# Kernel tuning notes

Hardware: AMD Instinct MI355X
Metric: run time of the kernel (lower is better)

Reference implementation:

```python
import jax, jax.numpy as jnp
import numpy as np

N, E, D, H, G = 50000, 640000, 128, 128, 64
EPS = 1e-5


def gcn_conv(x, row, col, W, b, n):
    # PyG GCNConv: linear transform, symmetric deg^-1/2 normalization (self-loops
    # already appended to row/col), scatter-add aggregation, then bias.
    h = x @ W  # [N, H]
    ones = jnp.ones(row.shape[0], dtype=h.dtype)
    deg = jax.ops.segment_sum(ones, col, num_segments=n)
    dinv = jnp.where(deg > 0, jax.lax.rsqrt(deg), 0.0)
    norm = dinv[row] * dinv[col]                       # [E+N]
    msg = h[row] * norm[:, None]                       # gather + scale
    out = jax.ops.segment_sum(msg, col, num_segments=n)  # scatter-add
    return out + b


def graph_layernorm(x, w, b):
    # PyG LayerNorm(mode='graph') with batch=None: normalize over the whole tensor.
    mu = x.mean()
    xc = x - mu
    std = jnp.sqrt((xc * xc).mean())
    return xc / (std + EPS) * w + b


def setup_inputs() -> dict:
    key = jax.random.key(0)
    ks = jax.random.split(key, 12)
    x = jax.random.normal(ks[0], (N, D), dtype=jnp.float32)
    edge_index = jax.random.randint(ks[1], (2, E), 0, N, dtype=jnp.int64)
    batch = jnp.sort(jax.random.randint(ks[2], (N,), 0, G, dtype=jnp.int64))
    s1 = 1.0 / np.sqrt(D)
    s2 = 1.0 / np.sqrt(H)
    return {
        "x": x,
        "edge_index": edge_index,
        "batch": batch,
        "W1": jax.random.normal(ks[3], (D, H), dtype=jnp.float32) * s1,
        "b1": jnp.zeros((H,), dtype=jnp.float32),
        "ln1_w": jnp.ones((H,), dtype=jnp.float32),
        "ln1_b": jnp.zeros((H,), dtype=jnp.float32),
        "W2": jax.random.normal(ks[4], (H, H), dtype=jnp.float32) * s2,
        "b2": jnp.zeros((H,), dtype=jnp.float32),
        "ln2_w": jnp.ones((H,), dtype=jnp.float32),
        "ln2_b": jnp.zeros((H,), dtype=jnp.float32),
        "fc_w": jax.random.normal(ks[5], (H, 1), dtype=jnp.float32) * s2,
        "fc_b": jnp.zeros((1,), dtype=jnp.float32),
    }


def reference(x, edge_index, batch, W1, b1, ln1_w, ln1_b, W2, b2, ln2_w, ln2_b, fc_w, fc_b):
    n = x.shape[0]
    loops = jnp.arange(n, dtype=edge_index.dtype)
    row = jnp.concatenate([edge_index[0], loops])  # add self-loops
    col = jnp.concatenate([edge_index[1], loops])

    h = gcn_conv(x, row, col, W1, b1, n)
    h = jax.nn.relu(graph_layernorm(h, ln1_w, ln1_b))
    h = gcn_conv(h, row, col, W2, b2, n)
    h = jax.nn.relu(graph_layernorm(h, ln2_w, ln2_b))

    # global_mean_pool over batch segment ids
    sums = jax.ops.segment_sum(h, batch, num_segments=G)          # [G, H]
    cnt = jax.ops.segment_sum(jnp.ones((n,), h.dtype), batch, num_segments=G)
    pooled = sums / jnp.maximum(cnt, 1.0)[:, None]

    logits = pooled @ fc_w + fc_b                                  # [G, 1]
    return jax.nn.sigmoid(logits).squeeze(-1)                      # [G]
```

## Files before the change

kernel.cpp:

```cpp
#include <hip/hip_runtime.h>
#include <math.h>

#define H 128
#define PC 16

typedef _Float16 half8v __attribute__((ext_vector_type(8)));
typedef float floatx4 __attribute__((ext_vector_type(4)));

__device__ __forceinline__ int lower_bound_i(const int* a, int n, int key) {
  int lo = 0, hi = n;
  while (lo < hi) { int mid = (lo + hi) >> 1; if (a[mid] < key) lo = mid + 1; else hi = mid; }
  return lo;
}

__global__ void k_initpack(const float* __restrict__ W1, const float* __restrict__ W2,
                           _Float16* __restrict__ PW1, _Float16* __restrict__ PW2,
                           int* cntE, float* slots, int* esrc, int cap, int n) {
  int b = blockIdx.x;
  int tid = threadIdx.x;
  if (b < 128) {
    int t = b * 256 + tid;
    const float* W = (t < 16384) ? W1 : W2;
    _Float16* PW = (t < 16384) ? PW1 : PW2;
    int u = t & 16383;
    int j = u & 7;
    int nn = (u >> 3) & 15;
    int quad = (u >> 7) & 3;
    int ks = (u >> 9) & 3;
    int ct = (u >> 11) & 7;
    PW[u] = (_Float16)W[(ks * 32 + quad * 8 + j) * H + ct * 16 + nn];
  } else {
    int i = (b - 128) * 256 + tid;
    int stride = 128 * 256;
    for (int j = i; j < n; j += stride) cntE[j] = 0;
    for (int j = i; j < 256; j += stride) slots[j] = 0.f;
    for (int j = i; j < cap; j += stride) esrc[j] = n;
  }
}

__global__ void k_count(const int* __restrict__ col, int* __restrict__ cntE,
                        int* __restrict__ perm, int E) {
  int e = blockIdx.x * blockDim.x + threadIdx.x;
  if (e < E) perm[e] = atomicAdd(&cntE[col[e]], 1);
}

__global__ void k_scan_block(const int* __restrict__ cnt, int* __restrict__ offs,
                             int* __restrict__ bsum, int n) {
  __shared__ int s[256];
  int tid = threadIdx.x;
  int i = blockIdx.x * 256 + tid;
  int v = (i < n) ? ((cnt[i] + 15) & ~15) : 0;
  s[tid] = v;
  __syncthreads();
  for (int d = 1; d < 256; d <<= 1) {
    int t = (tid >= d) ? s[tid - d] : 0;
    __syncthreads();
    s[tid] += t;
    __syncthreads();
  }
  if (i < n) offs[i] = s[tid] - v;
  if (tid == 255) bsum[blockIdx.x] = s[255];
}

__global__ void k_scan_add(int* __restrict__ offs, const int* __restrict__ bsum,
                           const int* __restrict__ cntE, float* __restrict__ dinv, int n) {
  __shared__ int sh[4];
  int tid = threadIdx.x;
  int v = (tid < blockIdx.x) ? bsum[tid] : 0;
#pragma unroll
  for (int o = 32; o > 0; o >>= 1) v += __shfl_xor(v, o, 64);
  if ((tid & 63) == 0) sh[tid >> 6] = v;
  __syncthreads();
  int boff = sh[0] + sh[1] + sh[2] + sh[3];
  int i = blockIdx.x * 256 + tid;
  if (i < n) {
    offs[i] += boff;
    dinv[i] = rsqrtf((float)(cntE[i] + 1));
  }
}

__device__ __forceinline__ void gemm_tile_f32(const float* __restrict__ Xf,
                                              const _Float16* __restrict__ PW,
                                              const float* __restrict__ dinv,
                                              _Float16* __restrict__ O,
                                              int wave, int laneid, int n) {
  int m = laneid & 15;
  int quad = laneid >> 4;
  int r0 = wave * 16;
  int row = r0 + m;
  if (row >= n) row = n - 1;
  floatx4 acc[8] = {};
  const half8v* PB8 = (const half8v*)PW;
#pragma unroll
  for (int ks = 0; ks < 4; ks++) {
    int kb = ks * 32 + quad * 8;
    const float* xr = Xf + (size_t)row * H + kb;
    float4 u0 = *(const float4*)xr;
    float4 u1 = *(const float4*)(xr + 4);
    half8v a;
    a[0] = (_Float16)u0.x; a[1] = (_Float16)u0.y; a[2] = (_Float16)u0.z; a[3] = (_Float16)u0.w;
    a[4] = (_Float16)u1.x; a[5] = (_Float16)u1.y; a[6] = (_Float16)u1.z; a[7] = (_Float16)u1.w;
#pragma unroll
    for (int ct = 0; ct < 8; ct++) {
      half8v b = PB8[((ct * 4 + ks) * 4 + quad) * 16 + m];
      acc[ct] = __builtin_amdgcn_mfma_f32_16x16x32_f16(a, b, acc[ct], 0, 0, 0);
    }
  }
  float dv[4];
#pragma unroll
  for (int reg = 0; reg < 4; reg++) {
    int ro = r0 + quad * 4 + reg;
    dv[reg] = (ro < n) ? dinv[ro] : 0.f;
  }
#pragma unroll
  for (int ct = 0; ct < 8; ct++) {
#pragma unroll
    for (int reg = 0; reg < 4; reg++) {
      int ro = r0 + quad * 4 + reg;
      if (ro < n) O[(size_t)ro * H + ct * 16 + m] = (_Float16)(acc[ct][reg] * dv[reg]);
    }
  }
}

__global__ __launch_bounds__(256) void k_sg1(const int* __restrict__ row, const int* __restrict__ col,
                                             const int* __restrict__ offs, const int* __restrict__ perm,
                                             int* __restrict__ esrc, int E,
                                             const float* __restrict__ Xf,
                                             const _Float16* __restrict__ PW,
                                             const float* __restrict__ dinv,
                                             _Float16* __restrict__ O, int n, int GB) {
  int b = blockIdx.x;
  if (b < GB) {
    if (b == 0 && threadIdx.x < 16) {
      half8v z = {};
      *(half8v*)&O[(size_t)n * H + threadIdx.x * 8] = z;
    }
    int wave = b * 4 + (threadIdx.x >> 6);
    int tiles = (n + 15) >> 4;
    if (wave >= tiles) return;
    gemm_tile_f32(Xf, PW, dinv, O, wave, threadIdx.x & 63, n);
  } else {
    int e = (b - GB) * 256 + threadIdx.x;
    if (e < E) {
      int c = col[e];
      esrc[offs[c] + perm[e]] = row[e];
    }
  }
}

__global__ __launch_bounds__(256) void k_gemm2(const _Float16* __restrict__ Xh,
                                               const _Float16* __restrict__ PW,
                                               const float* __restrict__ lnw,
                                               const float* __restrict__ lnb,
                                               const float* __restrict__ slot, float invM,
                                               const float* __restrict__ dinv,
                                               _Float16* __restrict__ O, int n) {
  if (blockIdx.x == 0 && threadIdx.x < 16) {
    half8v z = {};
    *(half8v*)&O[(size_t)n * H + threadIdx.x * 8] = z;
  }
  int wave = blockIdx.x * 4 + (threadIdx.x >> 6);
  int tiles = (n + 15) >> 4;
  if (wave >= tiles) return;
  int lane = threadIdx.x & 63;
  int m = lane & 15;
  int quad = lane >> 4;
  int r0 = wave * 16;
  int row = r0 + m;
  if (row >= n) row = n - 1;

  float s = slot[lane], q = slot[64 + lane];
#pragma unroll
  for (int o = 32; o > 0; o >>= 1) { s += __shfl_xor(s, o, 64); q += __shfl_xor(q, o, 64); }
  float mu = s * invM;
  float var = fmaxf(q * invM - mu * mu, 0.f);
  float rs = 1.f / (sqrtf(var) + 1e-5f);

  floatx4 acc[8] = {};
  const half8v* PB8 = (const half8v*)PW;
#pragma unroll
  for (int ks = 0; ks < 4; ks++) {
    int kb = ks * 32 + quad * 8;
    half8v hv = *(const half8v*)(Xh + (size_t)row * H + kb);
    float4 w0 = *(const float4*)(lnw + kb);
    float4 w1 = *(const float4*)(lnw + kb + 4);
    float4 c0 = *(const float4*)(lnb + kb);
    float4 c1 = *(const float4*)(lnb + kb + 4);
    half8v a;
    a[0] = (_Float16)fmaxf(((float)hv[0] - mu) * rs * w0.x + c0.x, 0.f);
    a[1] = (_Float16)fmaxf(((float)hv[1] - mu) * rs * w0.y + c0.y, 0.f);
    a[2] = (_Float16)fmaxf(((float)hv[2] - mu) * rs * w0.z + c0.z, 0.f);
    a[3] = (_Float16)fmaxf(((float)hv[3] - mu) * rs * w0.w + c0.w, 0.f);
    a[4] = (_Float16)fmaxf(((float)hv[4] - mu) * rs * w1.x + c1.x, 0.f);
    a[5] = (_Float16)fmaxf(((float)hv[5] - mu) * rs * w1.y + c1.y, 0.f);
    a[6] = (_Float16)fmaxf(((float)hv[6] - mu) * rs * w1.z + c1.z, 0.f);
    a[7] = (_Float16)fmaxf(((float)hv[7] - mu) * rs * w1.w + c1.w, 0.f);
#pragma unroll
    for (int ct = 0; ct < 8; ct++) {
      half8v b = PB8[((ct * 4 + ks) * 4 + quad) * 16 + m];
      acc[ct] = __builtin_amdgcn_mfma_f32_16x16x32_f16(a, b, acc[ct], 0, 0, 0);
    }
  }
  float dv[4];
#pragma unroll
  for (int reg = 0; reg < 4; reg++) {
    int ro = r0 + quad * 4 + reg;
    dv[reg] = (ro < n) ? dinv[ro] : 0.f;
  }
#pragma unroll
  for (int ct = 0; ct < 8; ct++) {
#pragma unroll
    for (int reg = 0; reg < 4; reg++) {
      int ro = r0 + quad * 4 + reg;
      if (ro < n) O[(size_t)ro * H + ct * 16 + m] = (_Float16)(acc[ct][reg] * dv[reg]);
    }
  }
}

__global__ __launch_bounds__(256) void k_agg(const _Float16* __restrict__ Gs,
                                             _Float16* __restrict__ Out,
                                             const int* __restrict__ esrc, const int* __restrict__ offs,
                                             const int* __restrict__ cntE, const float* __restrict__ dinv,
                                             const float* __restrict__ bias, float* __restrict__ slot,
                                             int n) {
  int sub = threadIdx.x >> 4;
  int lane = threadIdx.x & 15;
  int i = blockIdx.x * 16 + sub;
  float sv = 0.f, sq = 0.f;
  if (i < n) {
    float di = dinv[i];
    half8v gself = *(const half8v*)&Gs[(size_t)i * H + 8 * lane];
    float acc[8];
#pragma unroll
    for (int e = 0; e < 8; e++) acc[e] = (float)gself[e];
    int beg = offs[i];
    int c16 = (cntE[i] + 15) & ~15;
    int sid = (c16 > 0) ? esrc[beg + lane] : 0;
    for (int base = 0; base < c16; base += 16) {
      int cur = sid;
      if (base + 16 < c16) sid = esrc[beg + base + 16 + lane];
      int sg[16]; half8v hg[16];
#pragma unroll
      for (int u = 0; u < 16; u++) sg[u] = __shfl(cur, u, 16);
#pragma unroll
      for (int u = 0; u < 16; u++) hg[u] = *(const half8v*)&Gs[(size_t)sg[u] * H + 8 * lane];
#pragma unroll
      for (int e = 0; e < 8; e++) {
        float t0 = 0.f, t1 = 0.f;
#pragma unroll
        for (int u = 0; u < 8; u++) { t0 += (float)hg[u][e]; t1 += (float)hg[8 + u][e]; }
        acc[e] += t0 + t1;
      }
    }
    const float* bb = bias + 8 * lane;
    half8v vo;
#pragma unroll
    for (int e = 0; e < 8; e++) {
      float v = di * acc[e] + bb[e];
      vo[e] = (_Float16)v;
      sv += v;
      sq += v * v;
    }
    *(half8v*)&Out[(size_t)i * H + 8 * lane] = vo;
  }
#pragma unroll
  for (int o = 32; o > 0; o >>= 1) {
    sv += __shfl_xor(sv, o, 64);
    sq += __shfl_xor(sq, o, 64);
  }
  __shared__ float rsm[4], rqm[4];
  int wave = threadIdx.x >> 6;
  if ((threadIdx.x & 63) == 0) { rsm[wave] = sv; rqm[wave] = sq; }
  __syncthreads();
  if (threadIdx.x == 0) {
    float ts = rsm[0] + rsm[1] + rsm[2] + rsm[3];
    float tq = rqm[0] + rqm[1] + rqm[2] + rqm[3];
    int sl = blockIdx.x & 63;
    atomicAdd(&slot[sl], ts);
    atomicAdd(&slot[64 + sl], tq);
  }
}

__global__ __launch_bounds__(128) void k_pool(const _Float16* __restrict__ Hs,
                                              const int* __restrict__ batch,
                                              const float* __restrict__ lnw, const float* __restrict__ lnb,
                                              const float* __restrict__ slot, float invM,
                                              float* __restrict__ psum, int n) {
  int g = blockIdx.x / PC, q = blockIdx.x % PC;
  int t = threadIdx.x;
  int l = t & 63;
  float s = slot[l], qq = slot[64 + l];
#pragma unroll
  for (int o = 32; o > 0; o >>= 1) { s += __shfl_xor(s, o, 64); qq += __shfl_xor(qq, o, 64); }
  float mu = s * invM;
  float var = fmaxf(qq * invM - mu * mu, 0.f);
  float rs = 1.f / (sqrtf(var) + 1e-5f);

  int start = lower_bound_i(batch, n, g);
  int end = lower_bound_i(batch, n, g + 1);
  int tot = end - start;
  int per = (tot + PC - 1) / PC;
  int s0 = start + q * per;
  int e0 = s0 + per; if (e0 > end) e0 = end;
  float w = lnw[t], bb = lnb[t];
  float acc = 0.f;
  for (int i = s0; i < e0; i++) {
    float v = (float)Hs[(size_t)i * H + t];
    v = (v - mu) * rs * w + bb;
    acc += fmaxf(v, 0.f);
  }
  psum[(size_t)blockIdx.x * H + t] = acc;
}

__global__ __launch_bounds__(128) void k_fc(const float* __restrict__ psum, const int* __restrict__ batch,
                                            const float* __restrict__ fcw, const float* __restrict__ fcb,
                                            float* __restrict__ out, int n) {
  int g = blockIdx.x;
  int t = threadIdx.x;
  int start = lower_bound_i(batch, n, g);
  int end = lower_bound_i(batch, n, g + 1);
  float cnt = fmaxf((float)(end - start), 1.f);
  float tot = 0.f;
#pragma unroll
  for (int c = 0; c < PC; c++) tot += psum[(size_t)(g * PC + c) * H + t];
  float v = tot / cnt * fcw[t];
  int lane = t & 63, wave = t >> 6;
#pragma unroll
  for (int o = 32; o > 0; o >>= 1) v += __shfl_xor(v, o, 64);
  __shared__ float r2[2];
  if (lane == 0) r2[wave] = v;
  __syncthreads();
  if (t == 0) {
    float logit = r2[0] + r2[1] + fcb[0];
    out[g] = 1.f / (1.f + expf(-logit));
  }
}

extern "C" void kernel_launch(void* const* d_in, const int* in_sizes, int n_in,
                              void* d_out, int out_size, void* d_ws, size_t ws_size,
                              hipStream_t stream) {
  const float* x    = (const float*)d_in[0];
  const int*   ei   = (const int*)d_in[1];
  const int*   batch= (const int*)d_in[2];
  const float* W1   = (const float*)d_in[3];
  const float* b1   = (const float*)d_in[4];
  const float* ln1w = (const float*)d_in[5];
  const float* ln1b = (const float*)d_in[6];
  const float* W2   = (const float*)d_in[7];
  const float* b2   = (const float*)d_in[8];
  const float* ln2w = (const float*)d_in[9];
  const float* ln2b = (const float*)d_in[10];
  const float* fcw  = (const float*)d_in[11];
  const float* fcb  = (const float*)d_in[12];
  float* out = (float*)d_out;

  int N = in_sizes[2];
  int E = in_sizes[1] / 2;
  int G = out_size;
  int CAP = E + 15 * N;

  char* p = (char*)d_ws;
  int*   cntE   = (int*)p;   p += (size_t)N * 4;
  int*   offs   = (int*)p;   p += (size_t)N * 4;
  float* dinv   = (float*)p; p += (size_t)N * 4;
  int*   perm   = (int*)p;   p += (size_t)E * 4;
  int*   esrc   = (int*)p;   p += (size_t)CAP * 4;
  _Float16* bufA = (_Float16*)p; p += (size_t)(N + 1) * H * 2;
  _Float16* bufB = (_Float16*)p; p += (size_t)(N + 1) * H * 2;
  _Float16* PW1  = (_Float16*)p; p += 16384 * 2;
  _Float16* PW2  = (_Float16*)p; p += 16384 * 2;
  float* slots  = (float*)p; p += 256 * 4;
  int*   bsum   = (int*)p;   p += 256 * 4;
  float* psum   = (float*)p; p += (size_t)G * PC * H * 4;

  const int* row = ei;
  const int* col = ei + E;

  k_initpack<<<256, 256, 0, stream>>>(W1, W2, PW1, PW2, cntE, slots, esrc, CAP, N);
  int EB = (E + 255) / 256;
  k_count<<<EB, 256, 0, stream>>>(col, cntE, perm, E);
  int NB = (N + 255) / 256;
  k_scan_block<<<NB, 256, 0, stream>>>(cntE, offs, bsum, N);
  k_scan_add<<<NB, 256, 0, stream>>>(offs, bsum, cntE, dinv, N);

  int tiles = (N + 15) / 16;
  int GB = (tiles + 3) / 4;
  float invM = 1.f / ((float)N * (float)H);

  k_sg1<<<GB + EB, 256, 0, stream>>>(row, col, offs, perm, esrc, E, x, PW1, dinv, bufA, N, GB);
  k_agg<<<(N + 15) / 16, 256, 0, stream>>>(bufA, bufB, esrc, offs, cntE, dinv, b1, slots, N);
  k_gemm2<<<GB, 256, 0, stream>>>(bufB, PW2, ln1w, ln1b, slots, invM, dinv, bufA, N);
  k_agg<<<(N + 15) / 16, 256, 0, stream>>>(bufA, bufB, esrc, offs, cntE, dinv, b2, slots + 128, N);
  k_pool<<<G * PC, 128, 0, stream>>>(bufB, batch, ln2w, ln2b, slots + 128, invM, psum, N);
  k_fc<<<G, 128, 0, stream>>>(psum, batch, fcw, fcb, out, N);
}
```

Before: 254.6 us.

## Restructure CSR build with atomic allocation, fuse count into GEMM1, merge pool and fc

```diff
diff --git a/kernel.cpp b/kernel.cpp
--- a/kernel.cpp
+++ b/kernel.cpp
@@ -13,9 +13,11 @@
   return lo;
 }
 
-__global__ void k_initpack(const float* __restrict__ W1, const float* __restrict__ W2,
-                           _Float16* __restrict__ PW1, _Float16* __restrict__ PW2,
-                           int* cntE, float* slots, int* esrc, int cap, int n) {
+__global__ void k_init(const float* __restrict__ W1, const float* __restrict__ W2,
+                       _Float16* __restrict__ PW1, _Float16* __restrict__ PW2,
+                       int* cntE, float* slots, int* esrc,
+                       float* glog, int* gdone, int* total,
+                       int cap, int n, int g) {
   int b = blockIdx.x;
   int tid = threadIdx.x;
   if (b < 128) {
@@ -35,53 +37,13 @@
     for (int j = i; j < n; j += stride) cntE[j] = 0;
     for (int j = i; j < 256; j += stride) slots[j] = 0.f;
     for (int j = i; j < cap; j += stride) esrc[j] = n;
-  }
-}
-
-__global__ void k_count(const int* __restrict__ col, int* __restrict__ cntE,
-                        int* __restrict__ perm, int E) {
-  int e = blockIdx.x * blockDim.x + threadIdx.x;
-  if (e < E) perm[e] = atomicAdd(&cntE[col[e]], 1);
-}
-
-__global__ void k_scan_block(const int* __restrict__ cnt, int* __restrict__ offs,
-                             int* __restrict__ bsum, int n) {
-  __shared__ int s[256];
-  int tid = threadIdx.x;
-  int i = blockIdx.x * 256 + tid;
-  int v = (i < n) ? ((cnt[i] + 15) & ~15) : 0;
-  s[tid] = v;
-  __syncthreads();
-  for (int d = 1; d < 256; d <<= 1) {
-    int t = (tid >= d) ? s[tid - d] : 0;
-    __syncthreads();
-    s[tid] += t;
-    __syncthreads();
-  }
-  if (i < n) offs[i] = s[tid] - v;
-  if (tid == 255) bsum[blockIdx.x] = s[255];
-}
-
-__global__ void k_scan_add(int* __restrict__ offs, const int* __restrict__ bsum,
-                           const int* __restrict__ cntE, float* __restrict__ dinv, int n) {
-  __shared__ int sh[4];
-  int tid = threadIdx.x;
-  int v = (tid < blockIdx.x) ? bsum[tid] : 0;
-#pragma unroll
-  for (int o = 32; o > 0; o >>= 1) v += __shfl_xor(v, o, 64);
-  if ((tid & 63) == 0) sh[tid >> 6] = v;
-  __syncthreads();
-  int boff = sh[0] + sh[1] + sh[2] + sh[3];
-  int i = blockIdx.x * 256 + tid;
-  if (i < n) {
-    offs[i] += boff;
-    dinv[i] = rsqrtf((float)(cntE[i] + 1));
-  }
-}
-
-__device__ __forceinline__ void gemm_tile_f32(const float* __restrict__ Xf,
+    for (int j = i; j < g; j += stride) { glog[j] = 0.f; gdone[j] = 0; }
+    if (i == 0) *total = 0;
+  }
+}
+
+__device__ __forceinline__ void gemm_tile_raw(const float* __restrict__ Xf,
                                               const _Float16* __restrict__ PW,
-                                              const float* __restrict__ dinv,
                                               _Float16* __restrict__ O,
                                               int wave, int laneid, int n) {
   int m = laneid & 15;
@@ -106,29 +68,22 @@
       acc[ct] = __builtin_amdgcn_mfma_f32_16x16x32_f16(a, b, acc[ct], 0, 0, 0);
     }
   }
-  float dv[4];
-#pragma unroll
-  for (int reg = 0; reg < 4; reg++) {
-    int ro = r0 + quad * 4 + reg;
-    dv[reg] = (ro < n) ? dinv[ro] : 0.f;
-  }
 #pragma unroll
   for (int ct = 0; ct < 8; ct++) {
 #pragma unroll
     for (int reg = 0; reg < 4; reg++) {
       int ro = r0 + quad * 4 + reg;
-      if (ro < n) O[(size_t)ro * H + ct * 16 + m] = (_Float16)(acc[ct][reg] * dv[reg]);
-    }
-  }
-}
-
-__global__ __launch_bounds__(256) void k_sg1(const int* __restrict__ row, const int* __restrict__ col,
-                                             const int* __restrict__ offs, const int* __restrict__ perm,
-                                             int* __restrict__ esrc, int E,
-                                             const float* __restrict__ Xf,
+      if (ro < n) O[(size_t)ro * H + ct * 16 + m] = (_Float16)acc[ct][reg];
+    }
+  }
+}
+
+__global__ __launch_bounds__(256) void k_cg1(const float* __restrict__ Xf,
                                              const _Float16* __restrict__ PW,
-                                             const float* __restrict__ dinv,
-                                             _Float16* __restrict__ O, int n, int GB) {
+                                             _Float16* __restrict__ O,
+                                             const int* __restrict__ col,
+                                             int* __restrict__ cntE, int* __restrict__ perm,
+                                             int E, int n, int GB) {
   int b = blockIdx.x;
   if (b < GB) {
     if (b == 0 && threadIdx.x < 16) {
@@ -138,13 +93,108 @@
     int wave = b * 4 + (threadIdx.x >> 6);
     int tiles = (n + 15) >> 4;
     if (wave >= tiles) return;
-    gemm_tile_f32(Xf, PW, dinv, O, wave, threadIdx.x & 63, n);
+    gemm_tile_raw(Xf, PW, O, wave, threadIdx.x & 63, n);
   } else {
     int e = (b - GB) * 256 + threadIdx.x;
-    if (e < E) {
-      int c = col[e];
-      esrc[offs[c] + perm[e]] = row[e];
-    }
+    if (e < E) perm[e] = atomicAdd(&cntE[col[e]], 1);
+  }
+}
+
+__global__ void k_alloc(const int* __restrict__ cntE, int* __restrict__ offs,
+                        float* __restrict__ dinv, int* __restrict__ total, int n) {
+  int i = blockIdx.x * 256 + threadIdx.x;
+  if (i < n) {
+    int c = cntE[i];
+    offs[i] = atomicAdd(total, (c + 15) & ~15);
+    dinv[i] = rsqrtf((float)(c + 1));
+  } else if (i == n) {
+    dinv[n] = 0.f;
+  }
+}
+
+__global__ void k_scat(const int* __restrict__ row, const int* __restrict__ col,
+                       const int* __restrict__ offs, const int* __restrict__ perm,
+                       int* __restrict__ esrc, int E) {
+  int e = blockIdx.x * 256 + threadIdx.x;
+  if (e < E) esrc[offs[col[e]] + perm[e]] = row[e];
+}
+
+template<int WEIGHTED>
+__global__ __launch_bounds__(256) void k_agg(const _Float16* __restrict__ Gs,
+                                             _Float16* __restrict__ Out,
+                                             const int* __restrict__ esrc, const int* __restrict__ offs,
+                                             const int* __restrict__ cntE, const float* __restrict__ dinv,
+                                             const float* __restrict__ bias, float* __restrict__ slot,
+                                             int n) {
+  int sub = threadIdx.x >> 4;
+  int lane = threadIdx.x & 15;
+  int i = blockIdx.x * 16 + sub;
+  float sv = 0.f, sq = 0.f;
+  if (i < n) {
+    float di = dinv[i];
+    half8v gself = *(const half8v*)&Gs[(size_t)i * H + 8 * lane];
+    float acc[8];
+#pragma unroll
+    for (int e = 0; e < 8; e++) acc[e] = WEIGHTED ? di * (float)gself[e] : (float)gself[e];
+    int beg = offs[i];
+    int c16 = (cntE[i] + 15) & ~15;
+    int sid = (c16 > 0) ? esrc[beg + lane] : 0;
+    float dvp = WEIGHTED ? dinv[sid] : 0.f;
+    for (int base = 0; base < c16; base += 16) {
+      int cur = sid;
+      float dvc = dvp;
+      if (base + 16 < c16) {
+        sid = esrc[beg + base + 16 + lane];
+        if (WEIGHTED) dvp = dinv[sid];
+      }
+      int sg[16]; half8v hg[16]; float dg[16];
+#pragma unroll
+      for (int u = 0; u < 16; u++) sg[u] = __shfl(cur, u, 16);
+      if (WEIGHTED) {
+#pragma unroll
+        for (int u = 0; u < 16; u++) dg[u] = __shfl(dvc, u, 16);
+      }
+#pragma unroll
+      for (int u = 0; u < 16; u++) hg[u] = *(const half8v*)&Gs[(size_t)sg[u] * H + 8 * lane];
+#pragma unroll
+      for (int e = 0; e < 8; e++) {
+        float t0 = 0.f, t1 = 0.f;
+        if (WEIGHTED) {
+#pragma unroll
+          for (int u = 0; u < 8; u++) { t0 += dg[u] * (float)hg[u][e]; t1 += dg[8 + u] * (float)hg[8 + u][e]; }
+        } else {
+#pragma unroll
+          for (int u = 0; u < 8; u++) { t0 += (float)hg[u][e]; t1 += (float)hg[8 + u][e]; }
+        }
+        acc[e] += t0 + t1;
+      }
+    }
+    const float* bb = bias + 8 * lane;
+    half8v vo;
+#pragma unroll
+    for (int e = 0; e < 8; e++) {
+      float v = di * acc[e] + bb[e];
+      vo[e] = (_Float16)v;
+      sv += v;
+      sq += v * v;
+    }
+    *(half8v*)&Out[(size_t)i * H + 8 * lane] = vo;
+  }
+#pragma unroll
+  for (int o = 32; o > 0; o >>= 1) {
+    sv += __shfl_xor(sv, o, 64);
+    sq += __shfl_xor(sq, o, 64);
+  }
+  __shared__ float rsm[4], rqm[4];
+  int wave = threadIdx.x >> 6;
+  if ((threadIdx.x & 63) == 0) { rsm[wave] = sv; rqm[wave] = sq; }
+  __syncthreads();
+  if (threadIdx.x == 0) {
+    float ts = rsm[0] + rsm[1] + rsm[2] + rsm[3];
+    float tq = rqm[0] + rqm[1] + rqm[2] + rqm[3];
+    int sl = blockIdx.x & 63;
+    atomicAdd(&slot[sl], ts);
+    atomicAdd(&slot[64 + sl], tq);
   }
 }
 
@@ -217,75 +267,13 @@
   }
 }
 
-__global__ __launch_bounds__(256) void k_agg(const _Float16* __restrict__ Gs,
-                                             _Float16* __restrict__ Out,
-                                             const int* __restrict__ esrc, const int* __restrict__ offs,
-                                             const int* __restrict__ cntE, const float* __restrict__ dinv,
-                                             const float* __restrict__ bias, float* __restrict__ slot,
-                                             int n) {
-  int sub = threadIdx.x >> 4;
-  int lane = threadIdx.x & 15;
-  int i = blockIdx.x * 16 + sub;
-  float sv = 0.f, sq = 0.f;
-  if (i < n) {
-    float di = dinv[i];
-    half8v gself = *(const half8v*)&Gs[(size_t)i * H + 8 * lane];
-    float acc[8];
-#pragma unroll
-    for (int e = 0; e < 8; e++) acc[e] = (float)gself[e];
-    int beg = offs[i];
-    int c16 = (cntE[i] + 15) & ~15;
-    int sid = (c16 > 0) ? esrc[beg + lane] : 0;
-    for (int base = 0; base < c16; base += 16) {
-      int cur = sid;
-      if (base + 16 < c16) sid = esrc[beg + base + 16 + lane];
-      int sg[16]; half8v hg[16];
-#pragma unroll
-      for (int u = 0; u < 16; u++) sg[u] = __shfl(cur, u, 16);
-#pragma unroll
-      for (int u = 0; u < 16; u++) hg[u] = *(const half8v*)&Gs[(size_t)sg[u] * H + 8 * lane];
-#pragma unroll
-      for (int e = 0; e < 8; e++) {
-        float t0 = 0.f, t1 = 0.f;
-#pragma unroll
-        for (int u = 0; u < 8; u++) { t0 += (float)hg[u][e]; t1 += (float)hg[8 + u][e]; }
-        acc[e] += t0 + t1;
-      }
-    }
-    const float* bb = bias + 8 * lane;
-    half8v vo;
-#pragma unroll
-    for (int e = 0; e < 8; e++) {
-      float v = di * acc[e] + bb[e];
-      vo[e] = (_Float16)v;
-      sv += v;
-      sq += v * v;
-    }
-    *(half8v*)&Out[(size_t)i * H + 8 * lane] = vo;
-  }
-#pragma unroll
-  for (int o = 32; o > 0; o >>= 1) {
-    sv += __shfl_xor(sv, o, 64);
-    sq += __shfl_xor(sq, o, 64);
-  }
-  __shared__ float rsm[4], rqm[4];
-  int wave = threadIdx.x >> 6;
-  if ((threadIdx.x & 63) == 0) { rsm[wave] = sv; rqm[wave] = sq; }
-  __syncthreads();
-  if (threadIdx.x == 0) {
-    float ts = rsm[0] + rsm[1] + rsm[2] + rsm[3];
-    float tq = rqm[0] + rqm[1] + rqm[2] + rqm[3];
-    int sl = blockIdx.x & 63;
-    atomicAdd(&slot[sl], ts);
-    atomicAdd(&slot[64 + sl], tq);
-  }
-}
-
-__global__ __launch_bounds__(128) void k_pool(const _Float16* __restrict__ Hs,
-                                              const int* __restrict__ batch,
-                                              const float* __restrict__ lnw, const float* __restrict__ lnb,
-                                              const float* __restrict__ slot, float invM,
-                                              float* __restrict__ psum, int n) {
+__global__ __launch_bounds__(128) void k_poolfc(const _Float16* __restrict__ Hs,
+                                                const int* __restrict__ batch,
+                                                const float* __restrict__ lnw, const float* __restrict__ lnb,
+                                                const float* __restrict__ slot, float invM,
+                                                const float* __restrict__ fcw, const float* __restrict__ fcb,
+                                                float* __restrict__ glog, int* __restrict__ gdone,
+                                                float* __restrict__ out, int n) {
   int g = blockIdx.x / PC, q = blockIdx.x % PC;
   int t = threadIdx.x;
   int l = t & 63;
@@ -309,30 +297,23 @@
     v = (v - mu) * rs * w + bb;
     acc += fmaxf(v, 0.f);
   }
-  psum[(size_t)blockIdx.x * H + t] = acc;
-}
-
-__global__ __launch_bounds__(128) void k_fc(const float* __restrict__ psum, const int* __restrict__ batch,
-                                            const float* __restrict__ fcw, const float* __restrict__ fcb,
-                                            float* __restrict__ out, int n) {
-  int g = blockIdx.x;
-  int t = threadIdx.x;
-  int start = lower_bound_i(batch, n, g);
-  int end = lower_bound_i(batch, n, g + 1);
-  float cnt = fmaxf((float)(end - start), 1.f);
-  float tot = 0.f;
-#pragma unroll
-  for (int c = 0; c < PC; c++) tot += psum[(size_t)(g * PC + c) * H + t];
-  float v = tot / cnt * fcw[t];
-  int lane = t & 63, wave = t >> 6;
+  float cnt = fmaxf((float)tot, 1.f);
+  float v = acc * fcw[t] / cnt;
+  int wave = t >> 6;
 #pragma unroll
   for (int o = 32; o > 0; o >>= 1) v += __shfl_xor(v, o, 64);
   __shared__ float r2[2];
-  if (lane == 0) r2[wave] = v;
+  if (l == 0) r2[wave] = v;
   __syncthreads();
   if (t == 0) {
-    float logit = r2[0] + r2[1] + fcb[0];
-    out[g] = 1.f / (1.f + expf(-logit));
+    float part = r2[0] + r2[1];
+    atomicAdd(&glog[g], part);
+    __threadfence();
+    int old = atomicAdd(&gdone[g], 1);
+    if (old == PC - 1) {
+      float totv = atomicAdd(&glog[g], 0.0f);
+      out[g] = 1.f / (1.f + expf(-(totv + fcb[0])));
+    }
   }
 }
 
@@ -362,7 +343,7 @@
   char* p = (char*)d_ws;
   int*   cntE   = (int*)p;   p += (size_t)N * 4;
   int*   offs   = (int*)p;   p += (size_t)N * 4;
-  float* dinv   = (float*)p; p += (size_t)N * 4;
+  float* dinv   = (float*)p; p += (size_t)(N + 1) * 4;
   int*   perm   = (int*)p;   p += (size_t)E * 4;
   int*   esrc   = (int*)p;   p += (size_t)CAP * 4;
   _Float16* bufA = (_Float16*)p; p += (size_t)(N + 1) * H * 2;
@@ -370,27 +351,25 @@
   _Float16* PW1  = (_Float16*)p; p += 16384 * 2;
   _Float16* PW2  = (_Float16*)p; p += 16384 * 2;
   float* slots  = (float*)p; p += 256 * 4;
-  int*   bsum   = (int*)p;   p += 256 * 4;
-  float* psum   = (float*)p; p += (size_t)G * PC * H * 4;
+  float* glog   = (float*)p; p += (size_t)G * 4;
+  int*   gdone  = (int*)p;   p += (size_t)G * 4;
+  int*   total  = (int*)p;   p += 4;
 
   const int* row = ei;
   const int* col = ei + E;
 
-  k_initpack<<<256, 256, 0, stream>>>(W1, W2, PW1, PW2, cntE, slots, esrc, CAP, N);
   int EB = (E + 255) / 256;
-  k_count<<<EB, 256, 0, stream>>>(col, cntE, perm, E);
-  int NB = (N + 255) / 256;
-  k_scan_block<<<NB, 256, 0, stream>>>(cntE, offs, bsum, N);
-  k_scan_add<<<NB, 256, 0, stream>>>(offs, bsum, cntE, dinv, N);
-
   int tiles = (N + 15) / 16;
   int GB = (tiles + 3) / 4;
   float invM = 1.f / ((float)N * (float)H);
 
-  k_sg1<<<GB + EB, 256, 0, stream>>>(row, col, offs, perm, esrc, E, x, PW1, dinv, bufA, N, GB);
-  k_agg<<<(N + 15) / 16, 256, 0, stream>>>(bufA, bufB, esrc, offs, cntE, dinv, b1, slots, N);
+  k_init<<<256, 256, 0, stream>>>(W1, W2, PW1, PW2, cntE, slots, esrc, glog, gdone, total, CAP, N, G);
+  k_cg1<<<GB + EB, 256, 0, stream>>>(x, PW1, bufA, col, cntE, perm, E, N, GB);
+  k_alloc<<<(N + 1 + 255) / 256, 256, 0, stream>>>(cntE, offs, dinv, total, N);
+  k_scat<<<EB, 256, 0, stream>>>(row, col, offs, perm, esrc, E);
+  k_agg<1><<<(N + 15) / 16, 256, 0, stream>>>(bufA, bufB, esrc, offs, cntE, dinv, b1, slots, N);
   k_gemm2<<<GB, 256, 0, stream>>>(bufB, PW2, ln1w, ln1b, slots, invM, dinv, bufA, N);
-  k_agg<<<(N + 15) / 16, 256, 0, stream>>>(bufA, bufB, esrc, offs, cntE, dinv, b2, slots + 128, N);
-  k_pool<<<G * PC, 128, 0, stream>>>(bufB, batch, ln2w, ln2b, slots + 128, invM, psum, N);
-  k_fc<<<G, 128, 0, stream>>>(psum, batch, fcw, fcb, out, N);
-}
+  k_agg<0><<<(N + 15) / 16, 256, 0, stream>>>(bufA, bufB, esrc, offs, cntE, dinv, b2, slots + 128, N);
+  k_poolfc<<<G * PC, 128, 0, stream>>>(bufB, batch, ln2w, ln2b, slots + 128, invM, fcw, fcb,
+                                       glog, gdone, out, N);
+}
```

Result: slower. 280.7 us (+10.3%).

## Split feature buffers into four 32-column planes for cache-local aggregation

Applied to the files above, without the earlier changes.

```diff
diff --git a/kernel.cpp b/kernel.cpp
--- a/kernel.cpp
+++ b/kernel.cpp
@@ -12,6 +12,7 @@
   while (lo < hi) { int mid = (lo + hi) >> 1; if (a[mid] < key) lo = mid + 1; else hi = mid; }
   return lo;
 }
+
 
 __global__ void k_initpack(const float* __restrict__ W1, const float* __restrict__ W2,
                            _Float16* __restrict__ PW1, _Float16* __restrict__ PW2,
@@ -82,7 +83,7 @@
 __device__ __forceinline__ void gemm_tile_f32(const float* __restrict__ Xf,
                                               const _Float16* __restrict__ PW,
                                               const float* __restrict__ dinv,
-                                              _Float16* __restrict__ O,
+                                              _Float16* __restrict__ O, size_t PS,
                                               int wave, int laneid, int n) {
   int m = laneid & 15;
   int quad = laneid >> 4;
@@ -117,7 +118,9 @@
 #pragma unroll
     for (int reg = 0; reg < 4; reg++) {
       int ro = r0 + quad * 4 + reg;
-      if (ro < n) O[(size_t)ro * H + ct * 16 + m] = (_Float16)(acc[ct][reg] * dv[reg]);
+      if (ro < n)
+        O[(size_t)(ct >> 1) * PS + (size_t)ro * 32 + (ct & 1) * 16 + m] =
+            (_Float16)(acc[ct][reg] * dv[reg]);
     }
   }
 }
@@ -128,23 +131,88 @@
                                              const float* __restrict__ Xf,
                                              const _Float16* __restrict__ PW,
                                              const float* __restrict__ dinv,
-                                             _Float16* __restrict__ O, int n, int GB) {
+                                             _Float16* __restrict__ O, size_t PS, int n, int GB) {
   int b = blockIdx.x;
   if (b < GB) {
     if (b == 0 && threadIdx.x < 16) {
       half8v z = {};
-      *(half8v*)&O[(size_t)n * H + threadIdx.x * 8] = z;
+      int p = threadIdx.x >> 2, seg = threadIdx.x & 3;
+      *(half8v*)&O[(size_t)p * PS + (size_t)n * 32 + seg * 8] = z;
     }
     int wave = b * 4 + (threadIdx.x >> 6);
     int tiles = (n + 15) >> 4;
     if (wave >= tiles) return;
-    gemm_tile_f32(Xf, PW, dinv, O, wave, threadIdx.x & 63, n);
+    gemm_tile_f32(Xf, PW, dinv, O, PS, wave, threadIdx.x & 63, n);
   } else {
     int e = (b - GB) * 256 + threadIdx.x;
     if (e < E) {
       int c = col[e];
       esrc[offs[c] + perm[e]] = row[e];
     }
+  }
+}
+
+__global__ __launch_bounds__(256) void k_agg(const _Float16* __restrict__ Gs,
+                                             _Float16* __restrict__ Out,
+                                             const int* __restrict__ esrc, const int* __restrict__ offs,
+                                             const int* __restrict__ cntE, const float* __restrict__ dinv,
+                                             const float* __restrict__ bias, float* __restrict__ slot,
+                                             size_t PS, int n) {
+  int bid = blockIdx.x;
+  int p = (bid >> 1) & 3;
+  int u = (bid >> 3) * 2 + (bid & 1);
+  int nsub = threadIdx.x >> 2;
+  int lane = threadIdx.x & 3;
+  int i = u * 64 + nsub;
+  const _Float16* Gp = Gs + (size_t)p * PS;
+  float sv = 0.f, sq = 0.f;
+  if (i < n) {
+    float di = dinv[i];
+    half8v gself = *(const half8v*)&Gp[(size_t)i * 32 + 8 * lane];
+    float acc[8];
+#pragma unroll
+    for (int e = 0; e < 8; e++) acc[e] = (float)gself[e];
+    int beg = offs[i];
+    int c16 = (cntE[i] + 15) & ~15;
+    int sid = (c16 > 0) ? esrc[beg + lane] : 0;
+    for (int base = 0; base < c16; base += 4) {
+      int cur = sid;
+      if (base + 4 < c16) sid = esrc[beg + base + 4 + lane];
+      int sg[4]; half8v hg[4];
+#pragma unroll
+      for (int v = 0; v < 4; v++) sg[v] = __shfl(cur, v, 4);
+#pragma unroll
+      for (int v = 0; v < 4; v++) hg[v] = *(const half8v*)&Gp[(size_t)sg[v] * 32 + 8 * lane];
+#pragma unroll
+      for (int e = 0; e < 8; e++)
+        acc[e] += ((float)hg[0][e] + (float)hg[1][e]) + ((float)hg[2][e] + (float)hg[3][e]);
+    }
+    const float* bb = bias + p * 32 + 8 * lane;
+    half8v vo;
+#pragma unroll
+    for (int e = 0; e < 8; e++) {
+      float v = di * acc[e] + bb[e];
+      vo[e] = (_Float16)v;
+      sv += v;
+      sq += v * v;
+    }
+    *(half8v*)&Out[(size_t)p * PS + (size_t)i * 32 + 8 * lane] = vo;
+  }
+#pragma unroll
+  for (int o = 32; o > 0; o >>= 1) {
+    sv += __shfl_xor(sv, o, 64);
+    sq += __shfl_xor(sq, o, 64);
+  }
+  __shared__ float rsm[4], rqm[4];
+  int wave = threadIdx.x >> 6;
+  if ((threadIdx.x & 63) == 0) { rsm[wave] = sv; rqm[wave] = sq; }
+  __syncthreads();
+  if (threadIdx.x == 0) {
+    float ts = rsm[0] + rsm[1] + rsm[2] + rsm[3];
+    float tq = rqm[0] + rqm[1] + rqm[2] + rqm[3];
+    int sl = blockIdx.x & 63;
+    atomicAdd(&slot[sl], ts);
+    atomicAdd(&slot[64 + sl], tq);
   }
 }
 
@@ -154,10 +222,11 @@
                                                const float* __restrict__ lnb,
                                                const float* __restrict__ slot, float invM,
                                                const float* __restrict__ dinv,
-                                               _Float16* __restrict__ O, int n) {
+                                               _Float16* __restrict__ O, size_t PS, int n) {
   if (blockIdx.x == 0 && threadIdx.x < 16) {
     half8v z = {};
-    *(half8v*)&O[(size_t)n * H + threadIdx.x * 8] = z;
+    int p = threadIdx.x >> 2, seg = threadIdx.x & 3;
+    *(half8v*)&O[(size_t)p * PS + (size_t)n * 32 + seg * 8] = z;
   }
   int wave = blockIdx.x * 4 + (threadIdx.x >> 6);
   int tiles = (n + 15) >> 4;
@@ -181,7 +250,7 @@
 #pragma unroll
   for (int ks = 0; ks < 4; ks++) {
     int kb = ks * 32 + quad * 8;
-    half8v hv = *(const half8v*)(Xh + (size_t)row * H + kb);
+    half8v hv = *(const half8v*)(Xh + (size_t)ks * PS + (size_t)row * 32 + quad * 8);
     float4 w0 = *(const float4*)(lnw + kb);
     float4 w1 = *(const float4*)(lnw + kb + 4);
     float4 c0 = *(const float4*)(lnb + kb);
@@ -212,72 +281,10 @@
 #pragma unroll
     for (int reg = 0; reg < 4; reg++) {
       int ro = r0 + quad * 4 + reg;
-      if (ro < n) O[(size_t)ro * H + ct * 16 + m] = (_Float16)(acc[ct][reg] * dv[reg]);
-    }
-  }
-}
-
-__global__ __launch_bounds__(256) void k_agg(const _Float16* __restrict__ Gs,
-                                             _Float16* __restrict__ Out,
-                                             const int* __restrict__ esrc, const int* __restrict__ offs,
-                                             const int* __restrict__ cntE, const float* __restrict__ dinv,
-                                             const float* __restrict__ bias, float* __restrict__ slot,
-                                             int n) {
-  int sub = threadIdx.x >> 4;
-  int lane = threadIdx.x & 15;
-  int i = blockIdx.x * 16 + sub;
-  float sv = 0.f, sq = 0.f;
-  if (i < n) {
-    float di = dinv[i];
-    half8v gself = *(const half8v*)&Gs[(size_t)i * H + 8 * lane];
-    float acc[8];
-#pragma unroll
-    for (int e = 0; e < 8; e++) acc[e] = (float)gself[e];
-    int beg = offs[i];
-    int c16 = (cntE[i] + 15) & ~15;
-    int sid = (c16 > 0) ? esrc[beg + lane] : 0;
-    for (int base = 0; base < c16; base += 16) {
-      int cur = sid;
-      if (base + 16 < c16) sid = esrc[beg + base + 16 + lane];
-      int sg[16]; half8v hg[16];
-#pragma unroll
-      for (int u = 0; u < 16; u++) sg[u] = __shfl(cur, u, 16);
-#pragma unroll
-      for (int u = 0; u < 16; u++) hg[u] = *(const half8v*)&Gs[(size_t)sg[u] * H + 8 * lane];
-#pragma unroll
-      for (int e = 0; e < 8; e++) {
-        float t0 = 0.f, t1 = 0.f;
-#pragma unroll
-        for (int u = 0; u < 8; u++) { t0 += (float)hg[u][e]; t1 += (float)hg[8 + u][e]; }
-        acc[e] += t0 + t1;
-      }
-    }
-    const float* bb = bias + 8 * lane;
-    half8v vo;
-#pragma unroll
-    for (int e = 0; e < 8; e++) {
-      float v = di * acc[e] + bb[e];
-      vo[e] = (_Float16)v;
-      sv += v;
-      sq += v * v;
-    }
-    *(half8v*)&Out[(size_t)i * H + 8 * lane] = vo;
-  }
-#pragma unroll
-  for (int o = 32; o > 0; o >>= 1) {
-    sv += __shfl_xor(sv, o, 64);
-    sq += __shfl_xor(sq, o, 64);
-  }
-  __shared__ float rsm[4], rqm[4];
-  int wave = threadIdx.x >> 6;
-  if ((threadIdx.x & 63) == 0) { rsm[wave] = sv; rqm[wave] = sq; }
-  __syncthreads();
-  if (threadIdx.x == 0) {
-    float ts = rsm[0] + rsm[1] + rsm[2] + rsm[3];
-    float tq = rqm[0] + rqm[1] + rqm[2] + rqm[3];
-    int sl = blockIdx.x & 63;
-    atomicAdd(&slot[sl], ts);
-    atomicAdd(&slot[64 + sl], tq);
+      if (ro < n)
+        O[(size_t)(ct >> 1) * PS + (size_t)ro * 32 + (ct & 1) * 16 + m] =
+            (_Float16)(acc[ct][reg] * dv[reg]);
+    }
   }
 }
 
@@ -285,7 +292,7 @@
                                               const int* __restrict__ batch,
                                               const float* __restrict__ lnw, const float* __restrict__ lnb,
                                               const float* __restrict__ slot, float invM,
-                                              float* __restrict__ psum, int n) {
+                                              float* __restrict__ psum, size_t PS, int n) {
   int g = blockIdx.x / PC, q = blockIdx.x % PC;
   int t = threadIdx.x;
   int l = t & 63;
@@ -303,9 +310,10 @@
   int s0 = start + q * per;
   int e0 = s0 + per; if (e0 > end) e0 = end;
   float w = lnw[t], bb = lnb[t];
+  const _Float16* Hp = Hs + (size_t)(t >> 5) * PS + (t & 31);
   float acc = 0.f;
   for (int i = s0; i < e0; i++) {
-    float v = (float)Hs[(size_t)i * H + t];
+    float v = (float)Hp[(size_t)i * 32];
     v = (v - mu) * rs * w + bb;
     acc += fmaxf(v, 0.f);
   }
@@ -358,6 +366,7 @@
   int E = in_sizes[1] / 2;
   int G = out_size;
   int CAP = E + 15 * N;
+  size_t PS = (size_t)(N + 1) * 32;
 
   char* p = (char*)d_ws;
   int*   cntE   = (int*)p;   p += (size_t)N * 4;
@@ -387,10 +396,13 @@
   int GB = (tiles + 3) / 4;
   float invM = 1.f / ((float)N * (float)H);
 
-  k_sg1<<<GB + EB, 256, 0, stream>>>(row, col, offs, perm, esrc, E, x, PW1, dinv, bufA, N, GB);
-  k_agg<<<(N + 15) / 16, 256, 0, stream>>>(bufA, bufB, esrc, offs, cntE, dinv, b1, slots, N);
-  k_gemm2<<<GB, 256, 0, stream>>>(bufB, PW2, ln1w, ln1b, slots, invM, dinv, bufA, N);
-  k_agg<<<(N + 15) / 16, 256, 0, stream>>>(bufA, bufB, esrc, offs, cntE, dinv, b2, slots + 128, N);
-  k_pool<<<G * PC, 128, 0, stream>>>(bufB, batch, ln2w, ln2b, slots + 128, invM, psum, N);
+  int units = (N + 63) / 64;
+  int AGB = 8 * ((units + 1) / 2);
+
+  k_sg1<<<GB + EB, 256, 0, stream>>>(row, col, offs, perm, esrc, E, x, PW1, dinv, bufA, PS, N, GB);
+  k_agg<<<AGB, 256, 0, stream>>>(bufA, bufB, esrc, offs, cntE, dinv, b1, slots, PS, N);
+  k_gemm2<<<GB, 256, 0, stream>>>(bufB, PW2, ln1w, ln1b, slots, invM, dinv, bufA, PS, N);
+  k_agg<<<AGB, 256, 0, stream>>>(bufA, bufB, esrc, offs, cntE, dinv, b2, slots + 128, PS, N);
+  k_pool<<<G * PC, 128, 0, stream>>>(bufB, batch, ln2w, ln2b, slots + 128, invM, psum, PS, N);
   k_fc<<<G, 128, 0, stream>>>(psum, batch, fcw, fcb, out, N);
 }
```

After: 260.5 us. 1.02x slower.
